# Kernel optimization log

Hardware: AMD Instinct MI355X
Metric: run time of the kernel (lower is better)

## Reference

```python
import jax, jax.numpy as jnp
import numpy as np

WP = 1.0     # warp_penalty
TEMP = 0.01  # soft-min temperature
BIG = 1e7    # finite stand-in for +inf (exp(-BIG/TEMP) == 0 exactly in fp32)


def setup_inputs() -> dict:
    key = jax.random.key(0)
    k1, k2, k3, k4 = jax.random.split(key, 4)
    B, T1, T2, C = 8, 256, 1024, 128
    fea_a = jax.random.normal(k1, (B, T1, C), jnp.float32)
    fea_b = jax.random.normal(k2, (B, T2, C), jnp.float32)
    len_a = jax.random.randint(k3, (B,), T1 // 2, T1 + 1)
    len_b = jax.random.randint(k4, (B,), T2 // 2, T2 + 1)
    return {"fea_a": fea_a, "len_a": len_a, "fea_b": fea_b, "len_b": len_b}


def _softmin(v, temp):
    # v: [3, B, T1]; stable -temp*log(sum(exp(-v/temp)))
    m = jnp.min(v, axis=0)
    return m - temp * jnp.log(jnp.sum(jnp.exp(-(v - m) / temp), axis=0))


def _soft_dtw(fea_a, fea_b, len_a, len_b, wp=WP, temp=TEMP):
    B, T1, C = fea_a.shape
    T2 = fea_b.shape[1]
    # L1 cost: [B, T2, T1]  (rows index fea_b, cols index fea_a, as in torch code)
    cost = jnp.mean(jnp.abs(fea_a[:, None, :, :] - fea_b[:, :, None, :]), axis=-1)
    # skewed cost: skew[b, d, j] = cost[b, clip(d-j, 0, T2-1), j]
    D = T1 + T2 - 1
    d = jnp.arange(D)[:, None]
    j = jnp.arange(T1)[None, :]
    idx = jnp.clip(d - j, 0, T2 - 1)           # [D, T1]
    skew = cost[:, idx, j]                      # [B, D, T1]
    skew = jnp.swapaxes(skew, 0, 1)             # [D, B, T1] for scan

    pc0 = jnp.full((B, T1 + 1), BIG, jnp.float32)       # path_cost (diag d-1)
    pcp0 = pc0.at[:, 0].set(0.0)                         # path_cost_prev (diag d-2)

    def step(carry, crow):
        pc, pcp = carry
        dirs = jnp.stack([pcp[:, :-1], pc[:, 1:] + wp, pc[:, :-1] + wp], axis=0)
        new = crow + _softmin(dirs, temp)                # [B, T1]
        new = jnp.concatenate([jnp.full((B, 1), BIG, new.dtype), new], axis=1)
        return (new, pc), new

    _, ys = jax.lax.scan(step, (pc0, pcp0), skew)        # ys: [D, B, T1+1]
    # per-sample answer: diagonal len_a+len_b-2, entry len_a
    di = len_a + len_b - 2
    loss_i = ys[di, jnp.arange(B), len_a]
    return jnp.sum(loss_i)  # reduction='mean' over a length-1 accumulator == sum


def reference(fea_a, len_a, fea_b, len_b):
    return _soft_dtw(fea_a, fea_b, len_a, len_b)
```

## Files before the change

### kernel.cpp

```cpp
#include <hip/hip_runtime.h>
#include <hip/hip_bf16.h>
#include <hip/hip_fp16.h>
#include <cstddef>
#include <cstdint>

#define BIGV 10000000.0f
#define WPV  1.0f

#define BATCH 8
#define T1N 256
#define T2N 1024
#define CN 128
#define DN 1279

#define FLAG_MAGIC 0x600D0000

typedef __attribute__((ext_vector_type(2))) _Float16 half2v;

__global__ __launch_bounds__(256) void cost_kernel(const float* __restrict__ A,
                                                   const float* __restrict__ Bf,
                                                   const int* __restrict__ lenA,
                                                   const int* __restrict__ lenB,
                                                   float* __restrict__ sk) {
    __shared__ char As[64 * 256];
    __shared__ char Bs[127 * 256];

    const int b  = blockIdx.z;
    const int d0 = blockIdx.y * 64;
    const int j0 = blockIdx.x * 64;
    const int tid = threadIdx.x;

    const int dEnd = lenA[b] + lenB[b] - 2;
    if (d0 > dEnd) return;

    const float* Ab = A  + (size_t)b * T1N * CN;
    const float* Bb = Bf + (size_t)b * T2N * CN;

    const int tj = tid & 15;
    const int td = tid >> 4;
    const int brow0 = td - tj + 63;
    const int rbase = d0 - j0 - 63;

#define SWB(row, g) (((row) << 8) + ((((g) + (row)) & 15) << 4))

    #pragma unroll
    for (int i = 0; i < 8; ++i) {
        int idx = tid + i * 256;
        int row = idx >> 5;
        int q   = idx & 31;
        float4 f = *(const float4*)(Ab + (size_t)(j0 + row) * CN + (q << 2));
        half2v h0 = { (_Float16)f.x, (_Float16)f.y };
        half2v h1 = { (_Float16)f.z, (_Float16)f.w };
        char* dst = As + SWB(row, q >> 1) + ((q & 1) << 3);
        ((uint32_t*)dst)[0] = __builtin_bit_cast(uint32_t, h0);
        ((uint32_t*)dst)[1] = __builtin_bit_cast(uint32_t, h1);
    }
    #pragma unroll
    for (int i = 0; i < 16; ++i) {
        int idx = tid + i * 256;
        if (idx < 4064) {
            int row = idx >> 5;
            int q   = idx & 31;
            int gr = rbase + row;
            gr = gr < 0 ? 0 : (gr > T2N - 1 ? T2N - 1 : gr);
            float4 f = *(const float4*)(Bb + (size_t)gr * CN + (q << 2));
            half2v h0 = { (_Float16)f.x, (_Float16)f.y };
            half2v h1 = { (_Float16)f.z, (_Float16)f.w };
            char* dst = Bs + SWB(row, q >> 1) + ((q & 1) << 3);
            ((uint32_t*)dst)[0] = __builtin_bit_cast(uint32_t, h0);
            ((uint32_t*)dst)[1] = __builtin_bit_cast(uint32_t, h1);
        }
    }
    __syncthreads();

    float acc[4][4];
    #pragma unroll
    for (int i = 0; i < 4; ++i)
        #pragma unroll
        for (int j = 0; j < 4; ++j) acc[i][j] = 0.0f;

    const half2v one2 = { (_Float16)1.0f, (_Float16)1.0f };

    for (int g = 0; g < 16; ++g) {
        uint4 a4[4], bv[7];
        #pragma unroll
        for (int ji = 0; ji < 4; ++ji) {
            int row = tj + 16 * ji;
            a4[ji] = *(const uint4*)(As + SWB(row, g));
        }
        #pragma unroll
        for (int m = 0; m < 7; ++m) {
            int row = brow0 + 16 * (m - 3);
            bv[m] = *(const uint4*)(Bs + SWB(row, g));
        }
        #pragma unroll
        for (int dk = 0; dk < 4; ++dk) {
            #pragma unroll
            for (int ji = 0; ji < 4; ++ji) {
                uint4 au = a4[ji];
                uint4 bu = bv[dk - ji + 3];
                float a = acc[dk][ji];
                #pragma unroll
                for (int w = 0; w < 4; ++w) {
                    uint32_t ua = (&au.x)[w];
                    uint32_t ub = (&bu.x)[w];
                    half2v d2 = __builtin_bit_cast(half2v, ua)
                              - __builtin_bit_cast(half2v, ub);
                    uint32_t du = __builtin_bit_cast(uint32_t, d2) & 0x7FFF7FFFu;
#if __has_builtin(__builtin_amdgcn_fdot2)
                    a = __builtin_amdgcn_fdot2(__builtin_bit_cast(half2v, du),
                                               one2, a, false);
#else
                    half2v ad = __builtin_bit_cast(half2v, du);
                    a += (float)ad.x + (float)ad.y;
#endif
                }
                acc[dk][ji] = a;
            }
        }
    }
#undef SWB

    #pragma unroll
    for (int dk = 0; dk < 4; ++dk) {
        int d = d0 + td + 16 * dk;
        if (d < DN) {
            size_t rowoff = ((size_t)b * DN + d) * T1N;
            #pragma unroll
            for (int ji = 0; ji < 4; ++ji) {
                int j = j0 + tj + 16 * ji;
                sk[rowoff + j] = acc[dk][ji] * (1.0f / 128.0f);
            }
        }
    }
}

__device__ __forceinline__ float min3f(float a, float b, float c) {
    float d;
    asm("v_min3_f32 %0, %1, %2, %3" : "=v"(d) : "v"(a), "v"(b), "v"(c));
    return d;
}

__global__ __launch_bounds__(64, 1) void dp_reg_kernel(const float* __restrict__ sk,
                                                       const int* __restrict__ lenA,
                                                       const int* __restrict__ lenB,
                                                       float* __restrict__ partials,
                                                       int* __restrict__ flags,
                                                       float* __restrict__ out) {
    const int b = blockIdx.x;
    const int L = threadIdx.x;

    const int la = __builtin_amdgcn_readfirstlane(lenA[b]);
    const int lb = __builtin_amdgcn_readfirstlane(lenB[b]);
    const int dEnd = la + lb - 2;
    const int kLast = dEnd >> 4;

    const char* lanep = (const char*)(sk + (size_t)b * DN * T1N) + (L << 4);

    float v1_0 = BIGV, v1_1 = BIGV, v1_2 = BIGV, v1_3 = BIGV;
    float v2_0 = BIGV, v2_1 = BIGV, v2_2 = BIGV, v2_3 = BIGV;
    float p1_prev = (L == 0) ? 0.0f : BIGV;

    float4 A0, A1, A2, A3, A4, A5, A6, A7, A8, A9, A10, A11, A12, A13, A14, A15;
    float4 B0, B1, B2, B3, B4, B5, B6, B7, B8, B9, B10, B11, B12, B13, B14, B15;

#define SHFL_UP1(SRC)                                                       \
    __int_as_float(__builtin_amdgcn_update_dpp(                             \
        __float_as_int(BIGV), __float_as_int(SRC),                          \
        0x138 , 0xF, 0xF, false))

#define LOAD1(DST, KB, R) do {                                              \
        int row_ = ((KB) << 4) + (R);                                       \
        row_ = row_ > dEnd ? dEnd : row_;                                   \
        DST = *(const float4*)(lanep + (size_t)row_ * (T1N * 4));           \
    } while (0)

#define LOADALL(P, KB) do {                                                 \
        LOAD1(P##0, KB, 0);   LOAD1(P##1, KB, 1);   LOAD1(P##2, KB, 2);     \
        LOAD1(P##3, KB, 3);   LOAD1(P##4, KB, 4);   LOAD1(P##5, KB, 5);     \
        LOAD1(P##6, KB, 6);   LOAD1(P##7, KB, 7);   LOAD1(P##8, KB, 8);     \
        LOAD1(P##9, KB, 9);   LOAD1(P##10, KB, 10); LOAD1(P##11, KB, 11);   \
        LOAD1(P##12, KB, 12); LOAD1(P##13, KB, 13); LOAD1(P##14, KB, 14);   \
        LOAD1(P##15, KB, 15);                                               \
    } while (0)

#define DP_STEP(C4) do {                                                    \
        float4 c = (C4);                                                    \
        float p1 = SHFL_UP1(v1_3);                                          \
        float w0 = v1_0 + WPV, w1 = v1_1 + WPV;                             \
        float w2 = v1_2 + WPV, w3 = v1_3 + WPV;                             \
        float wp = p1 + WPV;                                                \
        float n0 = c.x + min3f(p1_prev, w0, wp);                            \
        float n1 = c.y + min3f(v2_0, w1, w0);                               \
        float n2 = c.z + min3f(v2_1, w2, w1);                               \
        float n3 = c.w + min3f(v2_2, w3, w2);                               \
        p1_prev = p1;                                                       \
        v2_0 = v1_0; v2_1 = v1_1; v2_2 = v1_2; v2_3 = v1_3;                 \
        v1_0 = n0;   v1_1 = n1;   v1_2 = n2;   v1_3 = n3;                   \
    } while (0)

#define DP_STEP_G(C4, R) do {                                               \
        float4 c = (C4);                                                    \
        float p1 = SHFL_UP1(v1_3);                                          \
        float w0 = v1_0 + WPV, w1 = v1_1 + WPV;                             \
        float w2 = v1_2 + WPV, w3 = v1_3 + WPV;                             \
        float wp = p1 + WPV;                                                \
        float n0 = c.x + min3f(p1_prev, w0, wp);                            \
        float n1 = c.y + min3f(v2_0, w1, w0);                               \
        float n2 = c.z + min3f(v2_1, w2, w1);                               \
        float n3 = c.w + min3f(v2_2, w3, w2);                               \
        if ((R) <= rem) {                                                   \
            p1_prev = p1;                                                   \
            v2_0 = v1_0; v2_1 = v1_1; v2_2 = v1_2; v2_3 = v1_3;             \
            v1_0 = n0;   v1_1 = n1;   v1_2 = n2;   v1_3 = n3;               \
        }                                                                   \
    } while (0)

#define STEP_RL(C4, KB, R) do { DP_STEP(C4); LOAD1(C4, KB, R); } while (0)

#define PROC_RELOAD(P, KB) do {                                             \
        STEP_RL(P##0, KB, 0);   STEP_RL(P##1, KB, 1);                       \
        STEP_RL(P##2, KB, 2);   STEP_RL(P##3, KB, 3);                       \
        STEP_RL(P##4, KB, 4);   STEP_RL(P##5, KB, 5);                       \
        STEP_RL(P##6, KB, 6);   STEP_RL(P##7, KB, 7);                       \
        STEP_RL(P##8, KB, 8);   STEP_RL(P##9, KB, 9);                       \
        STEP_RL(P##10, KB, 10); STEP_RL(P##11, KB, 11);                     \
        STEP_RL(P##12, KB, 12); STEP_RL(P##13, KB, 13);                     \
        STEP_RL(P##14, KB, 14); STEP_RL(P##15, KB, 15);                     \
    } while (0)

#define PROC_FULL(P) do {                                                   \
        DP_STEP(P##0);  DP_STEP(P##1);  DP_STEP(P##2);  DP_STEP(P##3);      \
        DP_STEP(P##4);  DP_STEP(P##5);  DP_STEP(P##6);  DP_STEP(P##7);      \
        DP_STEP(P##8);  DP_STEP(P##9);  DP_STEP(P##10); DP_STEP(P##11);     \
        DP_STEP(P##12); DP_STEP(P##13); DP_STEP(P##14); DP_STEP(P##15);     \
    } while (0)

#define PROC_GUARD(P) do {                                                  \
        DP_STEP_G(P##0, 0);   DP_STEP_G(P##1, 1);   DP_STEP_G(P##2, 2);     \
        DP_STEP_G(P##3, 3);   DP_STEP_G(P##4, 4);   DP_STEP_G(P##5, 5);     \
        DP_STEP_G(P##6, 6);   DP_STEP_G(P##7, 7);   DP_STEP_G(P##8, 8);     \
        DP_STEP_G(P##9, 9);   DP_STEP_G(P##10, 10); DP_STEP_G(P##11, 11);   \
        DP_STEP_G(P##12, 12); DP_STEP_G(P##13, 13); DP_STEP_G(P##14, 14);   \
        DP_STEP_G(P##15, 15);                                               \
    } while (0)

    LOADALL(A, 0);
    LOADALL(B, 1);

    int k = 0;
    while (k + 1 < kLast) {
        PROC_RELOAD(A, k + 2);
        PROC_RELOAD(B, k + 3);
        k += 2;
    }
    if (k < kLast) {
        PROC_FULL(A);
        const int rem = dEnd & 15;
        PROC_GUARD(B);
    } else {
        const int rem = dEnd & 15;
        PROC_GUARD(A);
    }

    const int tcap = la - 1;
    if (L == (tcap >> 2)) {
        const int kk = tcap & 3;
        float r = v1_0;
        if (kk == 1) r = v1_1;
        else if (kk == 2) r = v1_2;
        else if (kk == 3) r = v1_3;
        partials[b] = r;
        __threadfence();
        __hip_atomic_store(&flags[b], FLAG_MAGIC + b,
                           __ATOMIC_RELEASE, __HIP_MEMORY_SCOPE_AGENT);
    }

    if (b == 0 && L == 0) {
        float s = 0.0f;
        for (int i = 0; i < BATCH; ++i) {
            while (__hip_atomic_load(&flags[i], __ATOMIC_ACQUIRE,
                                     __HIP_MEMORY_SCOPE_AGENT) != FLAG_MAGIC + i)
                __builtin_amdgcn_s_sleep(2);
            s += __hip_atomic_load(&partials[i], __ATOMIC_RELAXED,
                                   __HIP_MEMORY_SCOPE_AGENT);
        }
        out[0] = s;
    }
#undef PROC_GUARD
#undef PROC_FULL
#undef PROC_RELOAD
#undef STEP_RL
#undef DP_STEP_G
#undef DP_STEP
#undef LOADALL
#undef LOAD1
#undef SHFL_UP1
}

extern "C" void kernel_launch(void* const* d_in, const int* in_sizes, int n_in,
                              void* d_out, int out_size, void* d_ws, size_t ws_size,
                              hipStream_t stream) {
    const float* feaA = (const float*)d_in[0];
    const int*   lenA = (const int*)d_in[1];
    const float* feaB = (const float*)d_in[2];
    const int*   lenB = (const int*)d_in[3];

    float* sk = (float*)d_ws;
    float* partials = (float*)((char*)d_ws + (size_t)BATCH * DN * T1N * sizeof(float));
    int*   flags    = (int*)(partials + BATCH);

    cost_kernel<<<dim3(T1N / 64, (DN + 63) / 64, BATCH), 256, 0, stream>>>(feaA, feaB, lenA, lenB, sk);
    dp_reg_kernel<<<BATCH, 64, 0, stream>>>(sk, lenA, lenB, partials, flags, (float*)d_out);
}
```

Baseline: 137.0 us.

## Fuse cost and DP kernels with per-tile flags for producer-consumer overlap

```diff
diff --git a/kernel.cpp b/kernel.cpp
--- a/kernel.cpp
+++ b/kernel.cpp
@@ -13,127 +13,11 @@
 #define CN 128
 #define DN 1279
 
+#define NTILES 640
 #define FLAG_MAGIC 0x600D0000
+#define TMAGIC     0x70000000
 
 typedef __attribute__((ext_vector_type(2))) _Float16 half2v;
-
-__global__ __launch_bounds__(256) void cost_kernel(const float* __restrict__ A,
-                                                   const float* __restrict__ Bf,
-                                                   const int* __restrict__ lenA,
-                                                   const int* __restrict__ lenB,
-                                                   float* __restrict__ sk) {
-    __shared__ char As[64 * 256];
-    __shared__ char Bs[127 * 256];
-
-    const int b  = blockIdx.z;
-    const int d0 = blockIdx.y * 64;
-    const int j0 = blockIdx.x * 64;
-    const int tid = threadIdx.x;
-
-    const int dEnd = lenA[b] + lenB[b] - 2;
-    if (d0 > dEnd) return;
-
-    const float* Ab = A  + (size_t)b * T1N * CN;
-    const float* Bb = Bf + (size_t)b * T2N * CN;
-
-    const int tj = tid & 15;
-    const int td = tid >> 4;
-    const int brow0 = td - tj + 63;
-    const int rbase = d0 - j0 - 63;
-
-#define SWB(row, g) (((row) << 8) + ((((g) + (row)) & 15) << 4))
-
-    #pragma unroll
-    for (int i = 0; i < 8; ++i) {
-        int idx = tid + i * 256;
-        int row = idx >> 5;
-        int q   = idx & 31;
-        float4 f = *(const float4*)(Ab + (size_t)(j0 + row) * CN + (q << 2));
-        half2v h0 = { (_Float16)f.x, (_Float16)f.y };
-        half2v h1 = { (_Float16)f.z, (_Float16)f.w };
-        char* dst = As + SWB(row, q >> 1) + ((q & 1) << 3);
-        ((uint32_t*)dst)[0] = __builtin_bit_cast(uint32_t, h0);
-        ((uint32_t*)dst)[1] = __builtin_bit_cast(uint32_t, h1);
-    }
-    #pragma unroll
-    for (int i = 0; i < 16; ++i) {
-        int idx = tid + i * 256;
-        if (idx < 4064) {
-            int row = idx >> 5;
-            int q   = idx & 31;
-            int gr = rbase + row;
-            gr = gr < 0 ? 0 : (gr > T2N - 1 ? T2N - 1 : gr);
-            float4 f = *(const float4*)(Bb + (size_t)gr * CN + (q << 2));
-            half2v h0 = { (_Float16)f.x, (_Float16)f.y };
-            half2v h1 = { (_Float16)f.z, (_Float16)f.w };
-            char* dst = Bs + SWB(row, q >> 1) + ((q & 1) << 3);
-            ((uint32_t*)dst)[0] = __builtin_bit_cast(uint32_t, h0);
-            ((uint32_t*)dst)[1] = __builtin_bit_cast(uint32_t, h1);
-        }
-    }
-    __syncthreads();
-
-    float acc[4][4];
-    #pragma unroll
-    for (int i = 0; i < 4; ++i)
-        #pragma unroll
-        for (int j = 0; j < 4; ++j) acc[i][j] = 0.0f;
-
-    const half2v one2 = { (_Float16)1.0f, (_Float16)1.0f };
-
-    for (int g = 0; g < 16; ++g) {
-        uint4 a4[4], bv[7];
-        #pragma unroll
-        for (int ji = 0; ji < 4; ++ji) {
-            int row = tj + 16 * ji;
-            a4[ji] = *(const uint4*)(As + SWB(row, g));
-        }
-        #pragma unroll
-        for (int m = 0; m < 7; ++m) {
-            int row = brow0 + 16 * (m - 3);
-            bv[m] = *(const uint4*)(Bs + SWB(row, g));
-        }
-        #pragma unroll
-        for (int dk = 0; dk < 4; ++dk) {
-            #pragma unroll
-            for (int ji = 0; ji < 4; ++ji) {
-                uint4 au = a4[ji];
-                uint4 bu = bv[dk - ji + 3];
-                float a = acc[dk][ji];
-                #pragma unroll
-                for (int w = 0; w < 4; ++w) {
-                    uint32_t ua = (&au.x)[w];
-                    uint32_t ub = (&bu.x)[w];
-                    half2v d2 = __builtin_bit_cast(half2v, ua)
-                              - __builtin_bit_cast(half2v, ub);
-                    uint32_t du = __builtin_bit_cast(uint32_t, d2) & 0x7FFF7FFFu;
-#if __has_builtin(__builtin_amdgcn_fdot2)
-                    a = __builtin_amdgcn_fdot2(__builtin_bit_cast(half2v, du),
-                                               one2, a, false);
-#else
-                    half2v ad = __builtin_bit_cast(half2v, du);
-                    a += (float)ad.x + (float)ad.y;
-#endif
-                }
-                acc[dk][ji] = a;
-            }
-        }
-    }
-#undef SWB
-
-    #pragma unroll
-    for (int dk = 0; dk < 4; ++dk) {
-        int d = d0 + td + 16 * dk;
-        if (d < DN) {
-            size_t rowoff = ((size_t)b * DN + d) * T1N;
-            #pragma unroll
-            for (int ji = 0; ji < 4; ++ji) {
-                int j = j0 + tj + 16 * ji;
-                sk[rowoff + j] = acc[dk][ji] * (1.0f / 128.0f);
-            }
-        }
-    }
-}
 
 __device__ __forceinline__ float min3f(float a, float b, float c) {
     float d;
@@ -141,28 +25,56 @@
     return d;
 }
 
-__global__ __launch_bounds__(64, 1) void dp_reg_kernel(const float* __restrict__ sk,
+__global__ __launch_bounds__(256, 1) void fused_kernel(const float* __restrict__ A,
+                                                       const float* __restrict__ Bf,
                                                        const int* __restrict__ lenA,
                                                        const int* __restrict__ lenB,
+                                                       float* __restrict__ sk,
+                                                       int* __restrict__ tflags,
                                                        float* __restrict__ partials,
-                                                       int* __restrict__ flags,
+                                                       int* __restrict__ bflags,
                                                        float* __restrict__ out) {
-    const int b = blockIdx.x;
-    const int L = threadIdx.x;
-
-    const int la = __builtin_amdgcn_readfirstlane(lenA[b]);
-    const int lb = __builtin_amdgcn_readfirstlane(lenB[b]);
-    const int dEnd = la + lb - 2;
-    const int kLast = dEnd >> 4;
-
-    const char* lanep = (const char*)(sk + (size_t)b * DN * T1N) + (L << 4);
-
-    float v1_0 = BIGV, v1_1 = BIGV, v1_2 = BIGV, v1_3 = BIGV;
-    float v2_0 = BIGV, v2_1 = BIGV, v2_2 = BIGV, v2_3 = BIGV;
-    float p1_prev = (L == 0) ? 0.0f : BIGV;
-
-    float4 A0, A1, A2, A3, A4, A5, A6, A7, A8, A9, A10, A11, A12, A13, A14, A15;
-    float4 B0, B1, B2, B3, B4, B5, B6, B7, B8, B9, B10, B11, B12, B13, B14, B15;
+    __shared__ char As[64 * 256];
+    __shared__ char Bs[127 * 256];
+
+    const int blk = blockIdx.x;
+    const int tid = threadIdx.x;
+
+    if (blk < BATCH) {
+        if (tid >= 64) return;
+        const int b = blk;
+        const int L = tid;
+
+        const int la = __builtin_amdgcn_readfirstlane(lenA[b]);
+        const int lb = __builtin_amdgcn_readfirstlane(lenB[b]);
+        const int dEnd = la + lb - 2;
+        const int kLast = dEnd >> 4;
+
+        const char* lanep = (const char*)(sk + (size_t)b * DN * T1N) + (L << 4);
+
+        float v1_0 = BIGV, v1_1 = BIGV, v1_2 = BIGV, v1_3 = BIGV;
+        float v2_0 = BIGV, v2_1 = BIGV, v2_2 = BIGV, v2_3 = BIGV;
+        float p1_prev = (L == 0) ? 0.0f : BIGV;
+
+        float4 A0, A1, A2, A3, A4, A5, A6, A7, A8, A9, A10, A11, A12, A13, A14, A15;
+        float4 B0, B1, B2, B3, B4, B5, B6, B7, B8, B9, B10, B11, B12, B13, B14, B15;
+
+        int g_done = -1;
+
+#define WAIT_GRPS(G) do {                                                   \
+        int gt_ = (G); gt_ = gt_ > 19 ? 19 : gt_;                           \
+        while (g_done < gt_) {                                              \
+            int gg = g_done + 1;                                            \
+            for (int x_ = 0; x_ < 4; ++x_) {                                \
+                int tt = (gg << 5) + (b << 2) + x_;                         \
+                while (__hip_atomic_load(&tflags[tt], __ATOMIC_ACQUIRE,     \
+                                         __HIP_MEMORY_SCOPE_AGENT)          \
+                       != TMAGIC + tt)                                      \
+                    __builtin_amdgcn_s_sleep(2);                            \
+            }                                                               \
+            g_done = gg;                                                    \
+        }                                                                   \
+    } while (0)
 
 #define SHFL_UP1(SRC)                                                       \
     __int_as_float(__builtin_amdgcn_update_dpp(                             \
@@ -245,48 +157,51 @@
         DP_STEP_G(P##15, 15);                                               \
     } while (0)
 
-    LOADALL(A, 0);
-    LOADALL(B, 1);
-
-    int k = 0;
-    while (k + 1 < kLast) {
-        PROC_RELOAD(A, k + 2);
-        PROC_RELOAD(B, k + 3);
-        k += 2;
-    }
-    if (k < kLast) {
-        PROC_FULL(A);
-        const int rem = dEnd & 15;
-        PROC_GUARD(B);
-    } else {
-        const int rem = dEnd & 15;
-        PROC_GUARD(A);
-    }
-
-    const int tcap = la - 1;
-    if (L == (tcap >> 2)) {
-        const int kk = tcap & 3;
-        float r = v1_0;
-        if (kk == 1) r = v1_1;
-        else if (kk == 2) r = v1_2;
-        else if (kk == 3) r = v1_3;
-        partials[b] = r;
-        __threadfence();
-        __hip_atomic_store(&flags[b], FLAG_MAGIC + b,
-                           __ATOMIC_RELEASE, __HIP_MEMORY_SCOPE_AGENT);
-    }
-
-    if (b == 0 && L == 0) {
-        float s = 0.0f;
-        for (int i = 0; i < BATCH; ++i) {
-            while (__hip_atomic_load(&flags[i], __ATOMIC_ACQUIRE,
-                                     __HIP_MEMORY_SCOPE_AGENT) != FLAG_MAGIC + i)
-                __builtin_amdgcn_s_sleep(2);
-            s += __hip_atomic_load(&partials[i], __ATOMIC_RELAXED,
-                                   __HIP_MEMORY_SCOPE_AGENT);
-        }
-        out[0] = s;
-    }
+        WAIT_GRPS(0);
+        LOADALL(A, 0);
+        LOADALL(B, 1);
+
+        int k = 0;
+        while (k + 1 < kLast) {
+            WAIT_GRPS((k + 3) >> 2);
+            PROC_RELOAD(A, k + 2);
+            PROC_RELOAD(B, k + 3);
+            k += 2;
+        }
+        if (k < kLast) {
+            PROC_FULL(A);
+            const int rem = dEnd & 15;
+            PROC_GUARD(B);
+        } else {
+            const int rem = dEnd & 15;
+            PROC_GUARD(A);
+        }
+
+        const int tcap = la - 1;
+        if (L == (tcap >> 2)) {
+            const int kk = tcap & 3;
+            float r = v1_0;
+            if (kk == 1) r = v1_1;
+            else if (kk == 2) r = v1_2;
+            else if (kk == 3) r = v1_3;
+            partials[b] = r;
+            __threadfence();
+            __hip_atomic_store(&bflags[b], FLAG_MAGIC + b,
+                               __ATOMIC_RELEASE, __HIP_MEMORY_SCOPE_AGENT);
+        }
+
+        if (b == 0 && L == 0) {
+            float s = 0.0f;
+            for (int i = 0; i < BATCH; ++i) {
+                while (__hip_atomic_load(&bflags[i], __ATOMIC_ACQUIRE,
+                                         __HIP_MEMORY_SCOPE_AGENT) != FLAG_MAGIC + i)
+                    __builtin_amdgcn_s_sleep(2);
+                s += __hip_atomic_load(&partials[i], __ATOMIC_RELAXED,
+                                       __HIP_MEMORY_SCOPE_AGENT);
+            }
+            out[0] = s;
+        }
+        return;
 #undef PROC_GUARD
 #undef PROC_FULL
 #undef PROC_RELOAD
@@ -296,6 +211,131 @@
 #undef LOADALL
 #undef LOAD1
 #undef SHFL_UP1
+#undef WAIT_GRPS
+    }
+
+    const int wid = blk - BATCH;
+
+    for (int t = wid; t < NTILES; t += 256) {
+        const int q  = t >> 5;
+        const int rr = t & 31;
+        const int tb = rr >> 2;
+        const int tx = rr & 3;
+        const int d0 = q << 6;
+        const int j0 = tx << 6;
+
+        const int dEnd = lenA[tb] + lenB[tb] - 2;
+
+        if (d0 <= dEnd) {
+            const float* Ab = A  + (size_t)tb * T1N * CN;
+            const float* Bb = Bf + (size_t)tb * T2N * CN;
+
+            const int tj = tid & 15;
+            const int td = tid >> 4;
+            const int brow0 = td - tj + 63;
+            const int rbase = d0 - j0 - 63;
+
+#define SWB(row, g) (((row) << 8) + ((((g) + (row)) & 15) << 4))
+
+            #pragma unroll
+            for (int i = 0; i < 8; ++i) {
+                int idx = tid + i * 256;
+                int row = idx >> 5;
+                int qq  = idx & 31;
+                float4 f = *(const float4*)(Ab + (size_t)(j0 + row) * CN + (qq << 2));
+                half2v h0 = { (_Float16)f.x, (_Float16)f.y };
+                half2v h1 = { (_Float16)f.z, (_Float16)f.w };
+                char* dst = As + SWB(row, qq >> 1) + ((qq & 1) << 3);
+                ((uint32_t*)dst)[0] = __builtin_bit_cast(uint32_t, h0);
+                ((uint32_t*)dst)[1] = __builtin_bit_cast(uint32_t, h1);
+            }
+            #pragma unroll
+            for (int i = 0; i < 16; ++i) {
+                int idx = tid + i * 256;
+                if (idx < 4064) {
+                    int row = idx >> 5;
+                    int qq  = idx & 31;
+                    int gr = rbase + row;
+                    gr = gr < 0 ? 0 : (gr > T2N - 1 ? T2N - 1 : gr);
+                    float4 f = *(const float4*)(Bb + (size_t)gr * CN + (qq << 2));
+                    half2v h0 = { (_Float16)f.x, (_Float16)f.y };
+                    half2v h1 = { (_Float16)f.z, (_Float16)f.w };
+                    char* dst = Bs + SWB(row, qq >> 1) + ((qq & 1) << 3);
+                    ((uint32_t*)dst)[0] = __builtin_bit_cast(uint32_t, h0);
+                    ((uint32_t*)dst)[1] = __builtin_bit_cast(uint32_t, h1);
+                }
+            }
+            __syncthreads();
+
+            float acc[4][4];
+            #pragma unroll
+            for (int i = 0; i < 4; ++i)
+                #pragma unroll
+                for (int j = 0; j < 4; ++j) acc[i][j] = 0.0f;
+
+            const half2v one2 = { (_Float16)1.0f, (_Float16)1.0f };
+
+            for (int g = 0; g < 16; ++g) {
+                uint4 a4[4], bv[7];
+                #pragma unroll
+                for (int ji = 0; ji < 4; ++ji) {
+                    int row = tj + 16 * ji;
+                    a4[ji] = *(const uint4*)(As + SWB(row, g));
+                }
+                #pragma unroll
+                for (int m = 0; m < 7; ++m) {
+                    int row = brow0 + 16 * (m - 3);
+                    bv[m] = *(const uint4*)(Bs + SWB(row, g));
+                }
+                #pragma unroll
+                for (int dk = 0; dk < 4; ++dk) {
+                    #pragma unroll
+                    for (int ji = 0; ji < 4; ++ji) {
+                        uint4 au = a4[ji];
+                        uint4 bu = bv[dk - ji + 3];
+                        float a = acc[dk][ji];
+                        #pragma unroll
+                        for (int w = 0; w < 4; ++w) {
+                            uint32_t ua = (&au.x)[w];
+                            uint32_t ub = (&bu.x)[w];
+                            half2v d2 = __builtin_bit_cast(half2v, ua)
+                                      - __builtin_bit_cast(half2v, ub);
+                            uint32_t du = __builtin_bit_cast(uint32_t, d2) & 0x7FFF7FFFu;
+#if __has_builtin(__builtin_amdgcn_fdot2)
+                            a = __builtin_amdgcn_fdot2(__builtin_bit_cast(half2v, du),
+                                                       one2, a, false);
+#else
+                            half2v ad = __builtin_bit_cast(half2v, du);
+                            a += (float)ad.x + (float)ad.y;
+#endif
+                        }
+                        acc[dk][ji] = a;
+                    }
+                }
+            }
+#undef SWB
+
+            #pragma unroll
+            for (int dk = 0; dk < 4; ++dk) {
+                int d = d0 + td + 16 * dk;
+                if (d < DN) {
+                    size_t rowoff = ((size_t)tb * DN + d) * T1N;
+                    #pragma unroll
+                    for (int ji = 0; ji < 4; ++ji) {
+                        int j = j0 + tj + 16 * ji;
+                        sk[rowoff + j] = acc[dk][ji] * (1.0f / 128.0f);
+                    }
+                }
+            }
+        }
+
+        __syncthreads();
+        if (tid == 0) {
+            __threadfence();
+            __hip_atomic_store(&tflags[t], TMAGIC + t,
+                               __ATOMIC_RELEASE, __HIP_MEMORY_SCOPE_AGENT);
+        }
+    }
 }
 
 extern "C" void kernel_launch(void* const* d_in, const int* in_sizes, int n_in,
@@ -306,10 +346,12 @@
     const float* feaB = (const float*)d_in[2];
     const int*   lenB = (const int*)d_in[3];
 
-    float* sk = (float*)d_ws;
+    float* sk       = (float*)d_ws;
     float* partials = (float*)((char*)d_ws + (size_t)BATCH * DN * T1N * sizeof(float));
-    int*   flags    = (int*)(partials + BATCH);
-
-    cost_kernel<<<dim3(T1N / 64, (DN + 63) / 64, BATCH), 256, 0, stream>>>(feaA, feaB, lenA, lenB, sk);
-    dp_reg_kernel<<<BATCH, 64, 0, stream>>>(sk, lenA, lenB, partials, flags, (float*)d_out);
+    int*   bflags   = (int*)(partials + BATCH);
+    int*   tflags   = bflags + BATCH;
+
+    fused_kernel<<<BATCH + 256, 256, 0, stream>>>(feaA, feaB, lenA, lenB,
+                                                  sk, tflags, partials, bflags,
+                                                  (float*)d_out);
 }
```

New measurement: 165.5 us. 1.21x slower.

## Triple-buffer DP row prefetch and ping-pong state registers

Applied to the files above, without the earlier changes.

```diff
diff --git a/kernel.cpp b/kernel.cpp
--- a/kernel.cpp
+++ b/kernel.cpp
@@ -141,12 +141,12 @@
     return d;
 }
 
-__global__ __launch_bounds__(64, 1) void dp_reg_kernel(const float* __restrict__ sk,
-                                                       const int* __restrict__ lenA,
-                                                       const int* __restrict__ lenB,
-                                                       float* __restrict__ partials,
-                                                       int* __restrict__ flags,
-                                                       float* __restrict__ out) {
+__global__ __launch_bounds__(64, 1) void dp_reg3_kernel(const float* __restrict__ sk,
+                                                        const int* __restrict__ lenA,
+                                                        const int* __restrict__ lenB,
+                                                        float* __restrict__ partials,
+                                                        int* __restrict__ flags,
+                                                        float* __restrict__ out) {
     const int b = blockIdx.x;
     const int L = threadIdx.x;
 
@@ -155,121 +155,102 @@
     const int dEnd = la + lb - 2;
     const int kLast = dEnd >> 4;
 
-    const char* lanep = (const char*)(sk + (size_t)b * DN * T1N) + (L << 4);
-
-    float v1_0 = BIGV, v1_1 = BIGV, v1_2 = BIGV, v1_3 = BIGV;
-    float v2_0 = BIGV, v2_1 = BIGV, v2_2 = BIGV, v2_3 = BIGV;
-    float p1_prev = (L == 0) ? 0.0f : BIGV;
-
-    float4 A0, A1, A2, A3, A4, A5, A6, A7, A8, A9, A10, A11, A12, A13, A14, A15;
-    float4 B0, B1, B2, B3, B4, B5, B6, B7, B8, B9, B10, B11, B12, B13, B14, B15;
+    const char* base = (const char*)(sk + (size_t)b * DN * T1N);
+    const int lo = L << 4;
+
+    float x0 = BIGV, x1 = BIGV, x2 = BIGV, x3 = BIGV;
+    float y0 = BIGV, y1 = BIGV, y2 = BIGV, y3 = BIGV;
+    float pp = (L == 0) ? 0.0f : BIGV;
+
+    float4 A0, A1, A2, A3, A4c, A5, A6, A7, A8, A9, A10, A11, A12, A13, A14, A15;
+    float4 B0, B1, B2, B3, B4c, B5, B6, B7, B8, B9, B10, B11, B12, B13, B14, B15;
+    float4 C0, C1, C2, C3, C4c, C5, C6, C7, C8, C9, C10, C11, C12, C13, C14, C15;
 
 #define SHFL_UP1(SRC)                                                       \
     __int_as_float(__builtin_amdgcn_update_dpp(                             \
         __float_as_int(BIGV), __float_as_int(SRC),                          \
         0x138 , 0xF, 0xF, false))
 
-#define LOAD1(DST, KB, R) do {                                              \
-        int row_ = ((KB) << 4) + (R);                                       \
-        row_ = row_ > dEnd ? dEnd : row_;                                   \
-        DST = *(const float4*)(lanep + (size_t)row_ * (T1N * 4));           \
-    } while (0)
+#define LOAD1(DST, KB, R)                                                   \
+        DST = *(const float4*)(base + (((KB) << 14) + ((R) << 10)) + lo)
 
 #define LOADALL(P, KB) do {                                                 \
         LOAD1(P##0, KB, 0);   LOAD1(P##1, KB, 1);   LOAD1(P##2, KB, 2);     \
-        LOAD1(P##3, KB, 3);   LOAD1(P##4, KB, 4);   LOAD1(P##5, KB, 5);     \
+        LOAD1(P##3, KB, 3);   LOAD1(P##4c, KB, 4);  LOAD1(P##5, KB, 5);     \
         LOAD1(P##6, KB, 6);   LOAD1(P##7, KB, 7);   LOAD1(P##8, KB, 8);     \
         LOAD1(P##9, KB, 9);   LOAD1(P##10, KB, 10); LOAD1(P##11, KB, 11);   \
         LOAD1(P##12, KB, 12); LOAD1(P##13, KB, 13); LOAD1(P##14, KB, 14);   \
         LOAD1(P##15, KB, 15);                                               \
     } while (0)
 
-#define DP_STEP(C4) do {                                                    \
-        float4 c = (C4);                                                    \
-        float p1 = SHFL_UP1(v1_3);                                          \
-        float w0 = v1_0 + WPV, w1 = v1_1 + WPV;                             \
-        float w2 = v1_2 + WPV, w3 = v1_3 + WPV;                             \
-        float wp = p1 + WPV;                                                \
-        float n0 = c.x + min3f(p1_prev, w0, wp);                            \
-        float n1 = c.y + min3f(v2_0, w1, w0);                               \
-        float n2 = c.z + min3f(v2_1, w2, w1);                               \
-        float n3 = c.w + min3f(v2_2, w3, w2);                               \
-        p1_prev = p1;                                                       \
-        v2_0 = v1_0; v2_1 = v1_1; v2_2 = v1_2; v2_3 = v1_3;                 \
-        v1_0 = n0;   v1_1 = n1;   v1_2 = n2;   v1_3 = n3;                   \
-    } while (0)
-
-#define DP_STEP_G(C4, R) do {                                               \
-        float4 c = (C4);                                                    \
-        float p1 = SHFL_UP1(v1_3);                                          \
-        float w0 = v1_0 + WPV, w1 = v1_1 + WPV;                             \
-        float w2 = v1_2 + WPV, w3 = v1_3 + WPV;                             \
-        float wp = p1 + WPV;                                                \
-        float n0 = c.x + min3f(p1_prev, w0, wp);                            \
-        float n1 = c.y + min3f(v2_0, w1, w0);                               \
-        float n2 = c.z + min3f(v2_1, w2, w1);                               \
-        float n3 = c.w + min3f(v2_2, w3, w2);                               \
-        if ((R) <= rem) {                                                   \
-            p1_prev = p1;                                                   \
-            v2_0 = v1_0; v2_1 = v1_1; v2_2 = v1_2; v2_3 = v1_3;             \
-            v1_0 = n0;   v1_1 = n1;   v1_2 = n2;   v1_3 = n3;               \
-        }                                                                   \
-    } while (0)
-
-#define STEP_RL(C4, KB, R) do { DP_STEP(C4); LOAD1(C4, KB, R); } while (0)
-
-#define PROC_RELOAD(P, KB) do {                                             \
-        STEP_RL(P##0, KB, 0);   STEP_RL(P##1, KB, 1);                       \
-        STEP_RL(P##2, KB, 2);   STEP_RL(P##3, KB, 3);                       \
-        STEP_RL(P##4, KB, 4);   STEP_RL(P##5, KB, 5);                       \
-        STEP_RL(P##6, KB, 6);   STEP_RL(P##7, KB, 7);                       \
-        STEP_RL(P##8, KB, 8);   STEP_RL(P##9, KB, 9);                       \
-        STEP_RL(P##10, KB, 10); STEP_RL(P##11, KB, 11);                     \
-        STEP_RL(P##12, KB, 12); STEP_RL(P##13, KB, 13);                     \
-        STEP_RL(P##14, KB, 14); STEP_RL(P##15, KB, 15);                     \
+#define DPP_STEP(C4, P, Q) do {                                             \
+        float4 c_ = (C4);                                                   \
+        float p1_ = SHFL_UP1(P##3);                                         \
+        float w0_ = P##0 + WPV, w1_ = P##1 + WPV;                           \
+        float w2_ = P##2 + WPV, w3_ = P##3 + WPV;                           \
+        float wp_ = p1_ + WPV;                                              \
+        float t0_ = c_.x + min3f(pp, w0_, wp_);                             \
+        float t1_ = c_.y + min3f(Q##0, w1_, w0_);                           \
+        float t2_ = c_.z + min3f(Q##1, w2_, w1_);                           \
+        float t3_ = c_.w + min3f(Q##2, w3_, w2_);                           \
+        pp = p1_;                                                           \
+        Q##0 = t0_; Q##1 = t1_; Q##2 = t2_; Q##3 = t3_;                     \
     } while (0)
 
 #define PROC_FULL(P) do {                                                   \
-        DP_STEP(P##0);  DP_STEP(P##1);  DP_STEP(P##2);  DP_STEP(P##3);      \
-        DP_STEP(P##4);  DP_STEP(P##5);  DP_STEP(P##6);  DP_STEP(P##7);      \
-        DP_STEP(P##8);  DP_STEP(P##9);  DP_STEP(P##10); DP_STEP(P##11);     \
-        DP_STEP(P##12); DP_STEP(P##13); DP_STEP(P##14); DP_STEP(P##15);     \
-    } while (0)
-
+        DPP_STEP(P##0,  x, y); DPP_STEP(P##1,  y, x);                       \
+        DPP_STEP(P##2,  x, y); DPP_STEP(P##3,  y, x);                       \
+        DPP_STEP(P##4c, x, y); DPP_STEP(P##5,  y, x);                       \
+        DPP_STEP(P##6,  x, y); DPP_STEP(P##7,  y, x);                       \
+        DPP_STEP(P##8,  x, y); DPP_STEP(P##9,  y, x);                       \
+        DPP_STEP(P##10, x, y); DPP_STEP(P##11, y, x);                       \
+        DPP_STEP(P##12, x, y); DPP_STEP(P##13, y, x);                       \
+        DPP_STEP(P##14, x, y); DPP_STEP(P##15, y, x);                       \
+    } while (0)
+
+#define GSTEP(C4, PN, QN, R) do { if ((R) <= rem) DPP_STEP(C4, PN, QN); } while (0)
 #define PROC_GUARD(P) do {                                                  \
-        DP_STEP_G(P##0, 0);   DP_STEP_G(P##1, 1);   DP_STEP_G(P##2, 2);     \
-        DP_STEP_G(P##3, 3);   DP_STEP_G(P##4, 4);   DP_STEP_G(P##5, 5);     \
-        DP_STEP_G(P##6, 6);   DP_STEP_G(P##7, 7);   DP_STEP_G(P##8, 8);     \
-        DP_STEP_G(P##9, 9);   DP_STEP_G(P##10, 10); DP_STEP_G(P##11, 11);   \
-        DP_STEP_G(P##12, 12); DP_STEP_G(P##13, 13); DP_STEP_G(P##14, 14);   \
-        DP_STEP_G(P##15, 15);                                               \
+        GSTEP(P##0,  x, y, 0);  GSTEP(P##1,  y, x, 1);                      \
+        GSTEP(P##2,  x, y, 2);  GSTEP(P##3,  y, x, 3);                      \
+        GSTEP(P##4c, x, y, 4);  GSTEP(P##5,  y, x, 5);                      \
+        GSTEP(P##6,  x, y, 6);  GSTEP(P##7,  y, x, 7);                      \
+        GSTEP(P##8,  x, y, 8);  GSTEP(P##9,  y, x, 9);                      \
+        GSTEP(P##10, x, y, 10); GSTEP(P##11, y, x, 11);                     \
+        GSTEP(P##12, x, y, 12); GSTEP(P##13, y, x, 13);                     \
+        GSTEP(P##14, x, y, 14); GSTEP(P##15, y, x, 15);                     \
     } while (0)
 
     LOADALL(A, 0);
     LOADALL(B, 1);
+    LOADALL(C, 2);
 
     int k = 0;
-    while (k + 1 < kLast) {
-        PROC_RELOAD(A, k + 2);
-        PROC_RELOAD(B, k + 3);
-        k += 2;
-    }
-    if (k < kLast) {
+    while (k + 2 < kLast) {
         PROC_FULL(A);
-        const int rem = dEnd & 15;
-        PROC_GUARD(B);
-    } else {
-        const int rem = dEnd & 15;
-        PROC_GUARD(A);
-    }
+        if (k + 3 <= kLast) LOADALL(A, k + 3);
+        PROC_FULL(B);
+        if (k + 4 <= kLast) LOADALL(B, k + 4);
+        PROC_FULL(C);
+        if (k + 5 <= kLast) LOADALL(C, k + 5);
+        k += 3;
+    }
+
+    const int rem = dEnd & 15;
+    if (kLast - k == 2)      { PROC_FULL(A); PROC_FULL(B); PROC_GUARD(C); }
+    else if (kLast - k == 1) { PROC_FULL(A); PROC_GUARD(B); }
+    else                     { PROC_GUARD(A); }
+
+    float f0, f1, f2, f3;
+    if ((rem & 1) == 0) { f0 = y0; f1 = y1; f2 = y2; f3 = y3; }
+    else                { f0 = x0; f1 = x1; f2 = x2; f3 = x3; }
 
     const int tcap = la - 1;
     if (L == (tcap >> 2)) {
         const int kk = tcap & 3;
-        float r = v1_0;
-        if (kk == 1) r = v1_1;
-        else if (kk == 2) r = v1_2;
-        else if (kk == 3) r = v1_3;
+        float r = f0;
+        if (kk == 1) r = f1;
+        else if (kk == 2) r = f2;
+        else if (kk == 3) r = f3;
         partials[b] = r;
         __threadfence();
         __hip_atomic_store(&flags[b], FLAG_MAGIC + b,
@@ -288,11 +269,9 @@
         out[0] = s;
     }
 #undef PROC_GUARD
+#undef GSTEP
 #undef PROC_FULL
-#undef PROC_RELOAD
-#undef STEP_RL
-#undef DP_STEP_G
-#undef DP_STEP
+#undef DPP_STEP
 #undef LOADALL
 #undef LOAD1
 #undef SHFL_UP1
@@ -306,10 +285,10 @@
     const float* feaB = (const float*)d_in[2];
     const int*   lenB = (const int*)d_in[3];
 
-    float* sk = (float*)d_ws;
+    float* sk       = (float*)d_ws;
     float* partials = (float*)((char*)d_ws + (size_t)BATCH * DN * T1N * sizeof(float));
     int*   flags    = (int*)(partials + BATCH);
 
     cost_kernel<<<dim3(T1N / 64, (DN + 63) / 64, BATCH), 256, 0, stream>>>(feaA, feaB, lenA, lenB, sk);
-    dp_reg_kernel<<<BATCH, 64, 0, stream>>>(sk, lenA, lenB, partials, flags, (float*)d_out);
-}
+    dp_reg3_kernel<<<BATCH, 64, 0, stream>>>(sk, lenA, lenB, partials, flags, (float*)d_out);
+}
```

New measurement: 131.8 us. -3.8%, faster.
